# Optimization experiments

Measured on AMD Instinct MI355X. Metric: run time of the kernel, lower is better.

Reference implementation:

```python
import jax, jax.numpy as jnp
import numpy as np

KERNEL_MUL = 2.0
KERNEL_NUM = 5
EPS = 1e-6
MU, SIGMA = 18.0, 8.0


def setup_inputs() -> dict:
    key = jax.random.key(0)
    k1, k2 = jax.random.split(key)
    N = 4096
    source = jax.random.uniform(k1, (N, 3), dtype=jnp.float32)
    target = jax.random.uniform(k2, (N, 3), dtype=jnp.float32)
    return {"source": source, "target": target}


def _confidence_weights(x):
    # x: [N, 3] columns (v, alpha, beta)
    v, alpha, beta = x[:, 0], x[:, 1], x[:, 2]
    phi = 2.0 * v + alpha + 1.0 / (beta + EPS)
    w = jnp.exp(-((phi - MU) ** 2) / (2.0 * SIGMA ** 2))
    w = w / (w.sum() + EPS)
    return jax.lax.stop_gradient(w)  # .detach() in torch


def reference(source, target):
    sw = _confidence_weights(source)
    tw = _confidence_weights(target)

    ns = source.shape[0]
    total = jnp.concatenate([source, target], axis=0)  # [2N, 3]
    n_total = total.shape[0]

    # pairwise squared L2 via the gram trick (same math as expand-subtract)
    sq = jnp.sum(total * total, axis=1)                      # [2N]
    L2 = sq[:, None] + sq[None, :] - 2.0 * (total @ total.T)  # [2N, 2N]

    # bandwidth from detached distances (torch uses L2_distance.data)
    bandwidth = jax.lax.stop_gradient(jnp.sum(L2)) / (n_total ** 2 - n_total)
    bandwidth = bandwidth / (KERNEL_MUL ** (KERNEL_NUM // 2))

    # the loss only touches the XY/YX cross blocks; YX = XY^T so their sums
    # are equal -> compute the kernel on the cross block only.
    L2_xy = L2[:ns, ns:]  # [ns, nt]
    kernel_xy = jnp.zeros_like(L2_xy)
    for i in range(KERNEL_NUM):
        kernel_xy = kernel_xy + jnp.exp(-L2_xy / (bandwidth * KERNEL_MUL ** i))

    weight_xy = sw[:, None] * tw[None, :]
    loss = -2.0 * jnp.sum(kernel_xy * weight_xy)  # -sum(XY) - sum(YX)
    return loss
```

## Files before the change

kernel.cpp:

```cpp
#include <hip/hip_runtime.h>
#include <math.h>

#define EPSF 1e-6f
#define MUF 18.0f
#define INV_2SIG2 (1.0f / 128.0f)

__device__ __forceinline__ float fexp2(float x) {
#if __has_builtin(__builtin_amdgcn_exp2f)
    return __builtin_amdgcn_exp2f(x);
#else
    return exp2f(x);
#endif
}

__global__ __launch_bounds__(256) void prep_kernel(
        const float* __restrict__ src, const float* __restrict__ tgt,
        int n, float4* __restrict__ pts, double* __restrict__ S) {
    int i = blockIdx.x * blockDim.x + threadIdx.x;
    double acc[6] = {0, 0, 0, 0, 0, 0};
    if (i < 2 * n) {
        const float* p = (i < n) ? (src + 3 * i) : (tgt + 3 * (i - n));
        float x = p[0], y = p[1], z = p[2];
        float phi = 2.0f * x + y + 1.0f / (z + EPSF);
        float dphi = phi - MUF;
        float w = expf(-(dphi * dphi) * INV_2SIG2);
        pts[i] = make_float4(x, y, z, w);
        float sq = x * x + y * y + z * z;
        acc[0] = (double)sq;
        acc[1] = (double)x;
        acc[2] = (double)y;
        acc[3] = (double)z;
        if (i < n) acc[4] = (double)w; else acc[5] = (double)w;
    }
    #pragma unroll
    for (int k = 0; k < 6; ++k) {
        double v = acc[k];
        for (int off = 32; off > 0; off >>= 1) v += __shfl_down(v, off);
        if ((threadIdx.x & 63) == 0) atomicAdd(&S[k], v);
    }
}

__global__ __launch_bounds__(256) void main_kernel(
        const float4* __restrict__ pts, int n,
        const double* __restrict__ S, double* __restrict__ partials) {
    double nt = 2.0 * (double)n;
    double sumL2 = 2.0 * nt * S[0] - 2.0 * (S[1] * S[1] + S[2] * S[2] + S[3] * S[3]);
    double bw = sumL2 / (nt * nt - nt);
    bw = bw * 0.25;
    float m = (float)(-1.4426950408889634 / bw);

    __shared__ float4 tg[64];
    int tid = threadIdx.x;
    int sIdx = blockIdx.x * 256 + tid;
    int tBase = n + blockIdx.y * 64;
    if (tid < 64) tg[tid] = pts[tBase + tid];
    __syncthreads();

    float4 sp = pts[sIdx];
    float a0 = 0.0f;
    #pragma unroll 4
    for (int j = 0; j < 64; ++j) {
        float4 t = tg[j];
        float dx = sp.x - t.x;
        float dy = sp.y - t.y;
        float dz = sp.z - t.z;
        float d = dx * dx + dy * dy + dz * dz;
        float u = d * m;
        float k = fexp2(u)
                + fexp2(u * 0.5f)
                + fexp2(u * 0.25f)
                + fexp2(u * 0.125f)
                + fexp2(u * 0.0625f);
        a0 += t.w * k;
    }
    float thread_sum = a0 * sp.w;

    double v = (double)thread_sum;
    for (int off = 32; off > 0; off >>= 1) v += __shfl_down(v, off);
    __shared__ double wsum[4];
    if ((tid & 63) == 0) wsum[tid >> 6] = v;
    __syncthreads();
    if (tid == 0) {
        partials[blockIdx.y * gridDim.x + blockIdx.x] =
            wsum[0] + wsum[1] + wsum[2] + wsum[3];
    }
}

__global__ __launch_bounds__(256) void fin_kernel(
        const double* __restrict__ S, const double* __restrict__ partials,
        int np, float* __restrict__ out) {
    int tid = threadIdx.x;
    double a = 0.0;
    for (int i = tid; i < np; i += 256) a += partials[i];
    for (int off = 32; off > 0; off >>= 1) a += __shfl_down(a, off);
    __shared__ double wsum[4];
    if ((tid & 63) == 0) wsum[tid >> 6] = a;
    __syncthreads();
    if (tid == 0) {
        double tot = wsum[0] + wsum[1] + wsum[2] + wsum[3];
        double denom = (S[4] + (double)EPSF) * (S[5] + (double)EPSF);
        out[0] = (float)(-2.0 * tot / denom);
    }
}

extern "C" void kernel_launch(void* const* d_in, const int* in_sizes, int n_in,
                              void* d_out, int out_size, void* d_ws, size_t ws_size,
                              hipStream_t stream) {
    const float* src = (const float*)d_in[0];
    const float* tgt = (const float*)d_in[1];
    int n = in_sizes[0] / 3;
    float* out = (float*)d_out;

    char* ws = (char*)d_ws;
    float4* pts = (float4*)ws;
    size_t off_S = (size_t)(2 * n) * sizeof(float4);
    double* S = (double*)(ws + off_S);
    double* partials = (double*)(ws + off_S + 8 * sizeof(double));

    int gx = (n + 255) / 256;
    int gy = (n + 63) / 64;
    int np = gx * gy;

    hipMemsetAsync(S, 0, 6 * sizeof(double), stream);
    prep_kernel<<<(2 * n + 255) / 256, 256, 0, stream>>>(src, tgt, n, pts, S);
    main_kernel<<<dim3(gx, gy), 256, 0, stream>>>(pts, n, S, partials);
    fin_kernel<<<1, 256, 0, stream>>>(S, partials, np, out);
}
```

Before: 82.73 us.

## Fuse prep, pairwise, and final reduction into one cooperative kernel with grid syncs

Replaces the memset plus three launches with one cooperative kernel of 256 blocks that uses grid.sync between the prep, pairwise-kernel and final-reduction phases. Global atomics give way to per-block partials, and target tiles grow from 64 to 256 points per block, so each block now covers a 256x256 tile. The aim is to remove launch and memset overhead. The cost is fewer blocks (256 instead of 1024), less latency hiding, and a hardcoded block count that assumes n=4096, with a fallback to three separate kernels if the cooperative launch fails.

```diff
diff --git a/kernel.cpp b/kernel.cpp
--- a/kernel.cpp
+++ b/kernel.cpp
@@ -1,106 +1,152 @@
 #include <hip/hip_runtime.h>
+#include <hip/hip_cooperative_groups.h>
 #include <math.h>
 
+namespace cg = cooperative_groups;
+
 #define EPSF 1e-6f
-#define MUF 18.0f
-#define INV_2SIG2 (1.0f / 128.0f)
 
 __device__ __forceinline__ float fexp2(float x) {
-#if __has_builtin(__builtin_amdgcn_exp2f)
     return __builtin_amdgcn_exp2f(x);
-#else
-    return exp2f(x);
-#endif
 }
 
-__global__ __launch_bounds__(256) void prep_kernel(
-        const float* __restrict__ src, const float* __restrict__ tgt,
-        int n, float4* __restrict__ pts, double* __restrict__ S) {
-    int i = blockIdx.x * blockDim.x + threadIdx.x;
-    double acc[6] = {0, 0, 0, 0, 0, 0};
-    if (i < 2 * n) {
-        const float* p = (i < n) ? (src + 3 * i) : (tgt + 3 * (i - n));
-        float x = p[0], y = p[1], z = p[2];
-        float phi = 2.0f * x + y + 1.0f / (z + EPSF);
-        float dphi = phi - MUF;
-        float w = expf(-(dphi * dphi) * INV_2SIG2);
-        pts[i] = make_float4(x, y, z, w);
-        float sq = x * x + y * y + z * z;
-        acc[0] = (double)sq;
-        acc[1] = (double)x;
-        acc[2] = (double)y;
-        acc[3] = (double)z;
-        if (i < n) acc[4] = (double)w; else acc[5] = (double)w;
-    }
+
+__device__ __forceinline__ void phaseA_body(
+        const float* __restrict__ src, const float* __restrict__ tgt, int n,
+        int i, int tid, float4* __restrict__ pts, double* __restrict__ prepP,
+        int pslot, double red[4][6]) {
+    const float* p = (i < n) ? (src + 3 * i) : (tgt + 3 * (i - n));
+    float x = p[0], y = p[1], z = p[2];
+    float phi = 2.f * x + y + 1.f / (z + EPSF);
+    float dphi = phi - 18.f;
+    float w = expf(-(dphi * dphi) * (1.f / 128.f));
+    pts[i] = make_float4(x, y, z, w);
+    double acc[6];
+    acc[0] = (double)(x * x + y * y + z * z);
+    acc[1] = (double)x; acc[2] = (double)y; acc[3] = (double)z;
+    acc[4] = (i < n) ? (double)w : 0.0;
+    acc[5] = (i < n) ? 0.0 : (double)w;
     #pragma unroll
     for (int k = 0; k < 6; ++k) {
         double v = acc[k];
         for (int off = 32; off > 0; off >>= 1) v += __shfl_down(v, off);
-        if ((threadIdx.x & 63) == 0) atomicAdd(&S[k], v);
+        if ((tid & 63) == 0) red[tid >> 6][k] = v;
     }
+    __syncthreads();
+    if (tid < 6)
+        prepP[pslot * 6 + tid] = red[0][tid] + red[1][tid] + red[2][tid] + red[3][tid];
 }
 
-__global__ __launch_bounds__(256) void main_kernel(
-        const float4* __restrict__ pts, int n,
-        const double* __restrict__ S, double* __restrict__ partials) {
-    double nt = 2.0 * (double)n;
-    double sumL2 = 2.0 * nt * S[0] - 2.0 * (S[1] * S[1] + S[2] * S[2] + S[3] * S[3]);
-    double bw = sumL2 / (nt * nt - nt);
-    bw = bw * 0.25;
-    float m = (float)(-1.4426950408889634 / bw);
+__device__ __forceinline__ float bw_scalar(const double* __restrict__ prepP, int n) {
+    double S0 = 0, Sx = 0, Sy = 0, Sz = 0;
+    for (int b = 0; b < 32; ++b) {
+        S0 += prepP[b * 6 + 0];
+        Sx += prepP[b * 6 + 1];
+        Sy += prepP[b * 6 + 2];
+        Sz += prepP[b * 6 + 3];
+    }
+    double ntf = 2.0 * (double)n;
+    double sumL2 = 2.0 * ntf * S0 - 2.0 * (Sx * Sx + Sy * Sy + Sz * Sz);
+    double bw = sumL2 / (ntf * ntf - ntf) * 0.25;
+    return (float)(-1.4426950408889634 / bw);
+}
 
-    __shared__ float4 tg[64];
-    int tid = threadIdx.x;
-    int sIdx = blockIdx.x * 256 + tid;
-    int tBase = n + blockIdx.y * 64;
-    if (tid < 64) tg[tid] = pts[tBase + tid];
+__device__ __forceinline__ double phaseB_body(
+        const float4* __restrict__ pts, int n, float m,
+        int bx, int by, int tid, float4* tg, double wsum[4]) {
+    tg[tid] = pts[n + (by << 8) + tid];
     __syncthreads();
-
-    float4 sp = pts[sIdx];
-    float a0 = 0.0f;
-    #pragma unroll 4
-    for (int j = 0; j < 64; ++j) {
+    float4 sp = pts[(bx << 8) + tid];
+    float a0 = 0.f;
+    #pragma unroll 8
+    for (int j = 0; j < 256; ++j) {
         float4 t = tg[j];
-        float dx = sp.x - t.x;
-        float dy = sp.y - t.y;
-        float dz = sp.z - t.z;
+        float dx = sp.x - t.x, dy = sp.y - t.y, dz = sp.z - t.z;
         float d = dx * dx + dy * dy + dz * dz;
         float u = d * m;
-        float k = fexp2(u)
-                + fexp2(u * 0.5f)
-                + fexp2(u * 0.25f)
-                + fexp2(u * 0.125f)
-                + fexp2(u * 0.0625f);
+        float k = fexp2(u) + fexp2(u * 0.5f) + fexp2(u * 0.25f)
+                + fexp2(u * 0.125f) + fexp2(u * 0.0625f);
         a0 += t.w * k;
     }
-    float thread_sum = a0 * sp.w;
-
-    double v = (double)thread_sum;
+    double v = (double)(a0 * sp.w);
     for (int off = 32; off > 0; off >>= 1) v += __shfl_down(v, off);
-    __shared__ double wsum[4];
     if ((tid & 63) == 0) wsum[tid >> 6] = v;
     __syncthreads();
-    if (tid == 0) {
-        partials[blockIdx.y * gridDim.x + blockIdx.x] =
-            wsum[0] + wsum[1] + wsum[2] + wsum[3];
-    }
+    return wsum[0] + wsum[1] + wsum[2] + wsum[3];
 }
 
-__global__ __launch_bounds__(256) void fin_kernel(
-        const double* __restrict__ S, const double* __restrict__ partials,
-        int np, float* __restrict__ out) {
-    int tid = threadIdx.x;
-    double a = 0.0;
-    for (int i = tid; i < np; i += 256) a += partials[i];
+__device__ __forceinline__ void phaseC_body(
+        const double* __restrict__ prepP, const double* __restrict__ mainP,
+        int tid, double wsum[4], float* __restrict__ out) {
+    double a = mainP[tid];
     for (int off = 32; off > 0; off >>= 1) a += __shfl_down(a, off);
-    __shared__ double wsum[4];
     if ((tid & 63) == 0) wsum[tid >> 6] = a;
     __syncthreads();
     if (tid == 0) {
         double tot = wsum[0] + wsum[1] + wsum[2] + wsum[3];
-        double denom = (S[4] + (double)EPSF) * (S[5] + (double)EPSF);
-        out[0] = (float)(-2.0 * tot / denom);
+        double Sw = 0, Tw = 0;
+        for (int b = 0; b < 32; ++b) {
+            Sw += prepP[b * 6 + 4];
+            Tw += prepP[b * 6 + 5];
+        }
+        out[0] = (float)(-2.0 * tot / ((Sw + (double)EPSF) * (Tw + (double)EPSF)));
     }
+}
+
+__global__ __launch_bounds__(256) void fused256(
+    const float* __restrict__ src, const float* __restrict__ tgt, int n,
+    float4* __restrict__ pts, double* __restrict__ prepP,
+    double* __restrict__ mainP, float* __restrict__ out)
+{
+    cg::grid_group grid = cg::this_grid();
+    const int tid = threadIdx.x;
+    const int bid = blockIdx.x;
+
+    __shared__ double red[4][6];
+    __shared__ float4 tg[256];
+    __shared__ double wsum[4];
+
+    if (bid < 32)
+        phaseA_body(src, tgt, n, bid * 256 + tid, tid, pts, prepP, bid, red);
+
+    grid.sync();
+
+    float m = bw_scalar(prepP, n);
+    double part = phaseB_body(pts, n, m, bid >> 4, bid & 15, tid, tg, wsum);
+    if (tid == 0) mainP[bid] = part;
+
+    grid.sync();
+
+    if (bid == 0) {
+        __syncthreads();
+        phaseC_body(prepP, mainP, tid, wsum, out);
+    }
+}
+
+__global__ __launch_bounds__(256) void prep2(
+    const float* __restrict__ src, const float* __restrict__ tgt, int n,
+    float4* __restrict__ pts, double* __restrict__ prepP) {
+    __shared__ double red[4][6];
+    phaseA_body(src, tgt, n, blockIdx.x * 256 + threadIdx.x, threadIdx.x,
+                pts, prepP, blockIdx.x, red);
+}
+
+__global__ __launch_bounds__(256) void main2(
+    const float4* __restrict__ pts, int n,
+    const double* __restrict__ prepP, double* __restrict__ mainP) {
+    __shared__ float4 tg[256];
+    __shared__ double wsum[4];
+    float m = bw_scalar(prepP, n);
+    double part = phaseB_body(pts, n, m, blockIdx.x, blockIdx.y,
+                              threadIdx.x, tg, wsum);
+    if (threadIdx.x == 0) mainP[blockIdx.y * 16 + blockIdx.x] = part;
+}
+
+__global__ __launch_bounds__(256) void fin2(
+    const double* __restrict__ prepP, const double* __restrict__ mainP,
+    float* __restrict__ out) {
+    __shared__ double wsum[4];
+    phaseC_body(prepP, mainP, threadIdx.x, wsum, out);
 }
 
 extern "C" void kernel_launch(void* const* d_in, const int* in_sizes, int n_in,
@@ -113,16 +159,19 @@
 
     char* ws = (char*)d_ws;
     float4* pts = (float4*)ws;
-    size_t off_S = (size_t)(2 * n) * sizeof(float4);
-    double* S = (double*)(ws + off_S);
-    double* partials = (double*)(ws + off_S + 8 * sizeof(double));
+    size_t off = (size_t)(2 * n) * sizeof(float4);
+    double* prepP = (double*)(ws + off);
+    off += 32 * 6 * sizeof(double);
+    double* mainP = (double*)(ws + off);
 
-    int gx = (n + 255) / 256;
-    int gy = (n + 63) / 64;
-    int np = gx * gy;
-
-    hipMemsetAsync(S, 0, 6 * sizeof(double), stream);
-    prep_kernel<<<(2 * n + 255) / 256, 256, 0, stream>>>(src, tgt, n, pts, S);
-    main_kernel<<<dim3(gx, gy), 256, 0, stream>>>(pts, n, S, partials);
-    fin_kernel<<<1, 256, 0, stream>>>(S, partials, np, out);
+    void* args[] = {(void*)&src, (void*)&tgt, (void*)&n, (void*)&pts,
+                    (void*)&prepP, (void*)&mainP, (void*)&out};
+    hipError_t e = hipLaunchCooperativeKernel((void*)fused256, dim3(256),
+                                              dim3(256), args, 0, stream);
+    if (e != hipSuccess) {
+        (void)hipGetLastError();
+        prep2<<<32, 256, 0, stream>>>(src, tgt, n, pts, prepP);
+        main2<<<dim3(16, 16), 256, 0, stream>>>(pts, n, prepP, mainP);
+        fin2<<<1, 256, 0, stream>>>(prepP, mainP, out);
+    }
 }
```

Result: slower. 129.2 us (+56.2%).
